# Optimization experiments

Measured on AMD Instinct MI355X. Metric: run time of the kernel, lower is better.

## Reference

```python
import jax, jax.numpy as jnp
import numpy as np
import math

D_MODEL = 1024
N_HEADS = 16
D_K = D_MODEL // N_HEADS


def setup_inputs() -> dict:
    key = jax.random.key(0)
    ks = jax.random.split(key, 12)
    B, S, D = 4, 2048, D_MODEL
    scale = 1.0 / math.sqrt(D)
    inp = {
        "q": jax.random.normal(ks[0], (B, S, D), jnp.float32),
        "k": jax.random.normal(ks[1], (B, S, D), jnp.float32),
        "v": jax.random.normal(ks[2], (B, S, D), jnp.float32),
        "w_q": jax.random.normal(ks[3], (D, D), jnp.float32) * scale,
        "b_q": jnp.zeros((D,), jnp.float32),
        "w_k": jax.random.normal(ks[4], (D, D), jnp.float32) * scale,
        "b_k": jnp.zeros((D,), jnp.float32),
        "w_v": jax.random.normal(ks[5], (D, D), jnp.float32) * scale,
        "b_v": jnp.zeros((D,), jnp.float32),
        "w_o": jax.random.normal(ks[6], (D, D), jnp.float32) * scale,
        "b_o": jnp.zeros((D,), jnp.float32),
        "ln_gamma": jnp.ones((D,), jnp.float32),
        "ln_beta": jnp.zeros((D,), jnp.float32),
    }
    return inp


def reference(q, k, v, w_q, b_q, w_k, b_k, w_v, b_v, w_o, b_o, ln_gamma, ln_beta):
    B, Sq, D = q.shape
    Sk = k.shape[1]
    residual = q
    # Projections (torch Linear: x @ W.T + b); split into heads -> [B, H, S, d_k]
    qh = (q @ w_q.T + b_q).reshape(B, Sq, N_HEADS, D_K).transpose(0, 2, 1, 3)
    kh = (k @ w_k.T + b_k).reshape(B, Sk, N_HEADS, D_K).transpose(0, 2, 1, 3)
    vh = (v @ w_v.T + b_v).reshape(B, Sk, N_HEADS, D_K).transpose(0, 2, 1, 3)
    # Scaled dot-product attention (dropout is identity in eval mode)
    scores = jnp.einsum("bhqd,bhkd->bhqk", qh, kh) / jnp.sqrt(jnp.float32(D_K))
    attn = jax.nn.softmax(scores, axis=-1)  # [B, H, Sq, Sk]
    ctx = jnp.einsum("bhqk,bhkd->bhqd", attn, vh)
    ctx = ctx.transpose(0, 2, 1, 3).reshape(B, Sq, D)
    out = ctx @ w_o.T + b_o
    # Post-LN with residual
    x = out + residual
    mu = jnp.mean(x, axis=-1, keepdims=True)
    var = jnp.var(x, axis=-1, keepdims=True)
    out = (x - mu) / jnp.sqrt(var + 1e-5) * ln_gamma + ln_beta
    return out, attn
```

## Files before the change

### kernel.cpp

```cpp
#include <hip/hip_runtime.h>

#define B_ 4
#define S_ 2048
#define D_ 1024
#define H_ 16
#define DK_ 64
#define M_ (B_ * S_)

typedef __attribute__((ext_vector_type(8))) _Float16 f16x8;
typedef __attribute__((ext_vector_type(4))) _Float16 f16x4;
typedef __attribute__((ext_vector_type(4))) float f32x4;

__device__ __forceinline__ f32x4 mfma16(f16x8 a, f16x8 b, f32x4 c) {
  return __builtin_amdgcn_mfma_f32_16x16x32_f16(a, b, c, 0, 0, 0);
}

__device__ __forceinline__ void gl2lds(const _Float16* g, _Float16* l) {
  __builtin_amdgcn_global_load_lds(
      (const __attribute__((address_space(1))) void*)g,
      (__attribute__((address_space(3))) void*)l, 16, 0, 0);
}

__global__ __launch_bounds__(256) void cvt8(const float* __restrict__ src,
                                            _Float16* __restrict__ dst, int n8) {
  const int i = blockIdx.x * 256 + threadIdx.x;
  if (i >= n8) return;
  const f32x4 a = *reinterpret_cast<const f32x4*>(&src[(size_t)i * 8]);
  const f32x4 b = *reinterpret_cast<const f32x4*>(&src[(size_t)i * 8 + 4]);
  f16x8 h;
  h[0] = (_Float16)a[0]; h[1] = (_Float16)a[1]; h[2] = (_Float16)a[2]; h[3] = (_Float16)a[3];
  h[4] = (_Float16)b[0]; h[5] = (_Float16)b[1]; h[6] = (_Float16)b[2]; h[7] = (_Float16)b[3];
  *reinterpret_cast<f16x8*>(&dst[(size_t)i * 8]) = h;
}

template <int MODE>
__global__ __launch_bounds__(256) void gemm_f16(const _Float16* __restrict__ A,
                                                const _Float16* __restrict__ Bw,
                                                const float* __restrict__ bias,
                                                void* __restrict__ Yv) {
  __shared__ _Float16 As[128 * 64];
  __shared__ _Float16 Bs[128 * 64];
  const int t = threadIdx.x;
  const int lane = t & 63;
  const int w = t >> 6;
  const int wr = w >> 1, wc = w & 1;
  const int l15 = lane & 15, g = lane >> 4;
  const int m0 = (blockIdx.x & 63) * 128;
  const int n0 = (blockIdx.x >> 6) * 128;

  f32x4 acc[4][4] = {};
  const int srow = lane >> 3;
  const int schk = (lane & 7) * 8;

  for (int kt = 0; kt < 16; ++kt) {
    const int k0 = kt * 64;
#pragma unroll
    for (int u = 0; u < 4; ++u) {
      const int r = u * 32 + w * 8 + srow;
      gl2lds(&A[(size_t)(m0 + r) * D_ + k0 + schk], &As[u * 2048 + w * 512]);
      gl2lds(&Bw[(size_t)(n0 + r) * D_ + k0 + schk], &Bs[u * 2048 + w * 512]);
    }
    __syncthreads();
#pragma unroll
    for (int kk = 0; kk < 2; ++kk) {
      f16x8 af[4], bfr[4];
#pragma unroll
      for (int m = 0; m < 4; ++m)
        af[m] = *reinterpret_cast<const f16x8*>(&As[(wr * 64 + m * 16 + l15) * 64 + kk * 32 + 8 * g]);
#pragma unroll
      for (int n = 0; n < 4; ++n)
        bfr[n] = *reinterpret_cast<const f16x8*>(&Bs[(wc * 64 + n * 16 + l15) * 64 + kk * 32 + 8 * g]);
#pragma unroll
      for (int m = 0; m < 4; ++m)
#pragma unroll
        for (int n = 0; n < 4; ++n)
          acc[m][n] = mfma16(af[m], bfr[n], acc[m][n]);
    }
    __syncthreads();
  }

  if constexpr (MODE == 0 || MODE == 1) {
    _Float16* Y = (_Float16*)Yv;
#pragma unroll
    for (int m = 0; m < 4; ++m)
#pragma unroll
      for (int n = 0; n < 4; ++n)
#pragma unroll
        for (int i = 0; i < 4; ++i) {
          const int R = m0 + wr * 64 + m * 16 + 4 * g + i;
          const int C = n0 + wc * 64 + n * 16 + l15;
          float val = acc[m][n][i] + bias[C];
          if constexpr (MODE == 1) val *= 0.125f;
          Y[(size_t)R * D_ + C] = (_Float16)val;
        }
  } else if constexpr (MODE == 2) {
    _Float16* Y = (_Float16*)Yv;
#pragma unroll
    for (int m = 0; m < 4; ++m)
#pragma unroll
      for (int n = 0; n < 4; ++n) {
        const int R0 = m0 + wr * 64 + m * 16 + 4 * g;
        const int C = n0 + wc * 64 + n * 16 + l15;
        const int b = R0 >> 11, s0 = R0 & (S_ - 1);
        const int h = C >> 6, dk = C & (DK_ - 1);
        f16x4 hv;
#pragma unroll
        for (int i = 0; i < 4; ++i) hv[i] = (_Float16)(acc[m][n][i] + bias[C]);
        *reinterpret_cast<f16x4*>(&Y[((size_t)((b * H_ + h) * DK_ + dk)) * S_ + s0]) = hv;
      }
  } else {
    float* Y = (float*)Yv;
#pragma unroll
    for (int m = 0; m < 4; ++m)
#pragma unroll
      for (int n = 0; n < 4; ++n)
#pragma unroll
        for (int i = 0; i < 4; ++i) {
          const int R = m0 + wr * 64 + m * 16 + 4 * g + i;
          const int C = n0 + wc * 64 + n * 16 + l15;
          Y[(size_t)R * D_ + C] = acc[m][n][i] + bias[C];
        }
  }
}

__global__ __launch_bounds__(256) void attn_pass1(const _Float16* __restrict__ Qh,
                                                  const _Float16* __restrict__ Kh,
                                                  float* __restrict__ lbuf) {
  __shared__ float red[4][64];
  const int t = threadIdx.x;
  const int lane = t & 63;
  const int w = t >> 6;
  const int l15 = lane & 15, g = lane >> 4;
  const int qc = blockIdx.x & 31;
  const int bh = blockIdx.x >> 5;
  const int b = bh >> 4, h = bh & 15;
  const int q0 = qc * 64;
  const _Float16* Qp = Qh + (size_t)b * S_ * D_ + h * DK_;
  const _Float16* Kp = Kh + (size_t)b * S_ * D_ + h * DK_;

  f16x8 qa[4][2];
#pragma unroll
  for (int mr = 0; mr < 4; ++mr)
#pragma unroll
    for (int kk = 0; kk < 2; ++kk)
      qa[mr][kk] = *reinterpret_cast<const f16x8*>(&Qp[(size_t)(q0 + mr * 16 + l15) * D_ + kk * 32 + 8 * g]);

  float l[4][4] = {};
  const int cbeg = w * (S_ / 4), cend = cbeg + (S_ / 4);
  for (int c0 = cbeg; c0 < cend; c0 += 16) {
    f16x8 kb0 = *reinterpret_cast<const f16x8*>(&Kp[(size_t)(c0 + l15) * D_ + 8 * g]);
    f16x8 kb1 = *reinterpret_cast<const f16x8*>(&Kp[(size_t)(c0 + l15) * D_ + 32 + 8 * g]);
#pragma unroll
    for (int mr = 0; mr < 4; ++mr) {
      f32x4 sc = {};
      sc = mfma16(qa[mr][0], kb0, sc);
      sc = mfma16(qa[mr][1], kb1, sc);
#pragma unroll
      for (int i = 0; i < 4; ++i) l[mr][i] += __expf(sc[i]);
    }
  }
#pragma unroll
  for (int mask = 1; mask < 16; mask <<= 1)
#pragma unroll
    for (int mr = 0; mr < 4; ++mr)
#pragma unroll
      for (int i = 0; i < 4; ++i) l[mr][i] += __shfl_xor(l[mr][i], mask, 64);
  if (l15 == 0)
#pragma unroll
    for (int mr = 0; mr < 4; ++mr)
#pragma unroll
      for (int i = 0; i < 4; ++i) red[w][mr * 16 + 4 * g + i] = l[mr][i];
  __syncthreads();
  if (t < 64)
    lbuf[(size_t)bh * S_ + q0 + t] = red[0][t] + red[1][t] + red[2][t] + red[3][t];
}

__global__ __launch_bounds__(256) void attn_pass2(const _Float16* __restrict__ Qh,
                                                  const _Float16* __restrict__ Kh,
                                                  const _Float16* __restrict__ Vt,
                                                  const float* __restrict__ lbuf,
                                                  float* __restrict__ attn,
                                                  _Float16* __restrict__ ctx) {
  __shared__ float Ps[4][32 * 36];
  const int t = threadIdx.x;
  const int lane = t & 63;
  const int w = t >> 6;
  const int l15 = lane & 15, g = lane >> 4;
  const int qc = blockIdx.x & 15;
  const int bh = blockIdx.x >> 4;
  const int b = bh >> 4, h = bh & 15;
  const int q0 = qc * 128 + w * 32;
  const _Float16* Qp = Qh + (size_t)b * S_ * D_ + h * DK_;
  const _Float16* Kp = Kh + (size_t)b * S_ * D_ + h * DK_;
  const _Float16* Vp = Vt + (size_t)bh * DK_ * S_;

  f16x8 qa[2][2];
#pragma unroll
  for (int mr = 0; mr < 2; ++mr)
#pragma unroll
    for (int kk = 0; kk < 2; ++kk)
      qa[mr][kk] = *reinterpret_cast<const f16x8*>(&Qp[(size_t)(q0 + mr * 16 + l15) * D_ + kk * 32 + 8 * g]);

  float il[2][4];
#pragma unroll
  for (int mr = 0; mr < 2; ++mr)
#pragma unroll
    for (int i = 0; i < 4; ++i)
      il[mr][i] = 1.0f / lbuf[(size_t)bh * S_ + q0 + mr * 16 + 4 * g + i];

  f32x4 accv[2][4] = {};
  float* Pw = Ps[w];
  const int sr = lane >> 3;
  const int sc4 = (lane & 7) * 4;

  for (int c0 = 0; c0 < S_; c0 += 32) {
#pragma unroll
    for (int ct = 0; ct < 2; ++ct) {
      const f16x8 kb0 = *reinterpret_cast<const f16x8*>(&Kp[(size_t)(c0 + ct * 16 + l15) * D_ + 8 * g]);
      const f16x8 kb1 = *reinterpret_cast<const f16x8*>(&Kp[(size_t)(c0 + ct * 16 + l15) * D_ + 32 + 8 * g]);
#pragma unroll
      for (int mr = 0; mr < 2; ++mr) {
        f32x4 sc = {};
        sc = mfma16(qa[mr][0], kb0, sc);
        sc = mfma16(qa[mr][1], kb1, sc);
#pragma unroll
        for (int i = 0; i < 4; ++i)
          Pw[(mr * 16 + 4 * g + i) * 36 + ct * 16 + l15] = __expf(sc[i]) * il[mr][i];
      }
    }
#pragma unroll
    for (int j = 0; j < 4; ++j) {
      const int r = sr + 8 * j;
      const f32x4 pv = *reinterpret_cast<const f32x4*>(&Pw[r * 36 + sc4]);
      __builtin_nontemporal_store(pv,
          reinterpret_cast<f32x4*>(&attn[((size_t)bh * S_ + q0 + r) * S_ + c0 + sc4]));
    }
#pragma unroll
    for (int mr = 0; mr < 2; ++mr) {
      const f32x4 p0 = *reinterpret_cast<const f32x4*>(&Pw[(mr * 16 + l15) * 36 + 8 * g]);
      const f32x4 p1 = *reinterpret_cast<const f32x4*>(&Pw[(mr * 16 + l15) * 36 + 8 * g + 4]);
      f16x8 pa;
#pragma unroll
      for (int j = 0; j < 4; ++j) { pa[j] = (_Float16)p0[j]; pa[4 + j] = (_Float16)p1[j]; }
#pragma unroll
      for (int n = 0; n < 4; ++n) {
        const f16x8 vb = *reinterpret_cast<const f16x8*>(&Vp[(size_t)(n * 16 + l15) * S_ + c0 + 8 * g]);
        accv[mr][n] = mfma16(pa, vb, accv[mr][n]);
      }
    }
  }
#pragma unroll
  for (int mr = 0; mr < 2; ++mr)
#pragma unroll
    for (int n = 0; n < 4; ++n)
#pragma unroll
      for (int i = 0; i < 4; ++i) {
        const int row = q0 + mr * 16 + 4 * g + i;
        ctx[((size_t)(b * S_ + row)) * D_ + h * DK_ + n * 16 + l15] = (_Float16)accv[mr][n][i];
      }
}

__global__ __launch_bounds__(256) void ln_kernel(float* __restrict__ out,
                                                 const float* __restrict__ resid,
                                                 const float* __restrict__ gamma,
                                                 const float* __restrict__ beta) {
  __shared__ float red[8];
  const int row = blockIdx.x;
  const int t = threadIdx.x;
  const int lane = t & 63, w = t >> 6;
  const size_t base = (size_t)row * D_ + t * 4;
  const f32x4 o = *reinterpret_cast<const f32x4*>(&out[base]);
  const f32x4 r = *reinterpret_cast<const f32x4*>(&resid[base]);
  const f32x4 x = o + r;
  float s = x[0] + x[1] + x[2] + x[3];
  float s2 = x[0] * x[0] + x[1] * x[1] + x[2] * x[2] + x[3] * x[3];
#pragma unroll
  for (int mask = 1; mask < 64; mask <<= 1) {
    s += __shfl_xor(s, mask, 64);
    s2 += __shfl_xor(s2, mask, 64);
  }
  if (lane == 0) { red[w] = s; red[w + 4] = s2; }
  __syncthreads();
  s = red[0] + red[1] + red[2] + red[3];
  s2 = red[4] + red[5] + red[6] + red[7];
  const float mu = s * (1.0f / D_);
  const float var = s2 * (1.0f / D_) - mu * mu;
  const float rstd = rsqrtf(var + 1e-5f);
  const f32x4 gm = *reinterpret_cast<const f32x4*>(&gamma[t * 4]);
  const f32x4 bt = *reinterpret_cast<const f32x4*>(&beta[t * 4]);
  f32x4 y;
#pragma unroll
  for (int j = 0; j < 4; ++j) y[j] = (x[j] - mu) * rstd * gm[j] + bt[j];
  *reinterpret_cast<f32x4*>(&out[base]) = y;
}

extern "C" void kernel_launch(void* const* d_in, const int* in_sizes, int n_in,
                              void* d_out, int out_size, void* d_ws, size_t ws_size,
                              hipStream_t stream) {
  (void)in_sizes; (void)n_in; (void)out_size; (void)ws_size;
  const float* q    = (const float*)d_in[0];
  const float* k    = (const float*)d_in[1];
  const float* v    = (const float*)d_in[2];
  const float* w_q  = (const float*)d_in[3];
  const float* b_q  = (const float*)d_in[4];
  const float* w_k  = (const float*)d_in[5];
  const float* b_k  = (const float*)d_in[6];
  const float* w_v  = (const float*)d_in[7];
  const float* b_v  = (const float*)d_in[8];
  const float* w_o  = (const float*)d_in[9];
  const float* b_o  = (const float*)d_in[10];
  const float* ln_g = (const float*)d_in[11];
  const float* ln_b = (const float*)d_in[12];

  char* ws = (char*)d_ws;
  _Float16* wq_h = (_Float16*)(ws + ((size_t)0 << 20));
  _Float16* wk_h = (_Float16*)(ws + ((size_t)2 << 20));
  _Float16* wv_h = (_Float16*)(ws + ((size_t)4 << 20));
  _Float16* wo_h = (_Float16*)(ws + ((size_t)6 << 20));
  _Float16* qf   = (_Float16*)(ws + ((size_t)8 << 20));
  _Float16* kf   = (_Float16*)(ws + ((size_t)26 << 20));
  _Float16* vf   = (_Float16*)(ws + ((size_t)44 << 20));
  _Float16* Qh   = (_Float16*)(ws + ((size_t)62 << 20));
  _Float16* Kh   = (_Float16*)(ws + ((size_t)80 << 20));
  _Float16* Vt   = (_Float16*)(ws + ((size_t)98 << 20));
  _Float16* ctx  = (_Float16*)(ws + ((size_t)116 << 20));
  float*    lbuf = (float*)(ws + ((size_t)134 << 20));

  float* out_f = (float*)d_out;
  float* attn_f = out_f + (size_t)M_ * D_;

  const int n8in = M_ * D_ / 8;
  const int n8w  = D_ * D_ / 8;
  cvt8<<<n8in / 256, 256, 0, stream>>>(q, qf, n8in);
  cvt8<<<n8in / 256, 256, 0, stream>>>(k, kf, n8in);
  cvt8<<<n8in / 256, 256, 0, stream>>>(v, vf, n8in);
  cvt8<<<n8w / 256, 256, 0, stream>>>(w_q, wq_h, n8w);
  cvt8<<<n8w / 256, 256, 0, stream>>>(w_k, wk_h, n8w);
  cvt8<<<n8w / 256, 256, 0, stream>>>(w_v, wv_h, n8w);
  cvt8<<<n8w / 256, 256, 0, stream>>>(w_o, wo_h, n8w);

  gemm_f16<1><<<512, 256, 0, stream>>>(qf, wq_h, b_q, Qh);
  gemm_f16<0><<<512, 256, 0, stream>>>(kf, wk_h, b_k, Kh);
  gemm_f16<2><<<512, 256, 0, stream>>>(vf, wv_h, b_v, Vt);

  attn_pass1<<<B_ * H_ * (S_ / 64), 256, 0, stream>>>(Qh, Kh, lbuf);
  attn_pass2<<<B_ * H_ * (S_ / 128), 256, 0, stream>>>(Qh, Kh, Vt, lbuf, attn_f, ctx);

  gemm_f16<3><<<512, 256, 0, stream>>>(ctx, wo_h, b_o, out_f);
  ln_kernel<<<M_, 256, 0, stream>>>(out_f, q, ln_g, ln_b);
}
```

Before: 541.2 us.

## Fuse softmax denominator pass into attention kernel and merge conversion launches

Folds the row-sum pass into the attention kernel: each wave first sweeps all keys to accumulate exp sums for its 32 query rows, then runs the existing probability/context pass, removing the separate kernel and the lbuf round trip. The seven fp32-to-fp16 conversion launches are merged into one indexed kernel. The Q scale now includes log2(e) so exp2f replaces __expf. The fused kernel has fewer blocks per row-sum sweep (32 rows per wave instead of 64 per block split across waves), so the first pass has less parallelism and more redundant K reads.

Result: slower. 614.6 us (+13.5%).

```diff
diff --git a/kernel.cpp b/kernel.cpp
--- a/kernel.cpp
+++ b/kernel.cpp
@@ -11,6 +11,8 @@
 typedef __attribute__((ext_vector_type(4))) _Float16 f16x4;
 typedef __attribute__((ext_vector_type(4))) float f32x4;
 
+#define QSCALE 0.18033688011113607f
+
 __device__ __forceinline__ f32x4 mfma16(f16x8 a, f16x8 b, f32x4 c) {
   return __builtin_amdgcn_mfma_f32_16x16x32_f16(a, b, c, 0, 0, 0);
 }
@@ -21,16 +23,37 @@
       (__attribute__((address_space(3))) void*)l, 16, 0, 0);
 }
 
-__global__ __launch_bounds__(256) void cvt8(const float* __restrict__ src,
-                                            _Float16* __restrict__ dst, int n8) {
+#define NIN8 (M_ * D_ / 8)
+#define NW8 (D_ * D_ / 8)
+__global__ __launch_bounds__(256) void cvt_all(
+    const float* __restrict__ q, const float* __restrict__ k, const float* __restrict__ v,
+    const float* __restrict__ wq, const float* __restrict__ wk, const float* __restrict__ wv,
+    const float* __restrict__ wo,
+    _Float16* __restrict__ qf, _Float16* __restrict__ kf, _Float16* __restrict__ vf,
+    _Float16* __restrict__ wqh, _Float16* __restrict__ wkh, _Float16* __restrict__ wvh,
+    _Float16* __restrict__ woh) {
   const int i = blockIdx.x * 256 + threadIdx.x;
-  if (i >= n8) return;
-  const f32x4 a = *reinterpret_cast<const f32x4*>(&src[(size_t)i * 8]);
-  const f32x4 b = *reinterpret_cast<const f32x4*>(&src[(size_t)i * 8 + 4]);
+  const float* src;
+  _Float16* dst;
+  int off;
+  if (i < 3 * NIN8) {
+    const int t = i >> 20;
+    off = i & (NIN8 - 1);
+    src = t == 0 ? q : (t == 1 ? k : v);
+    dst = t == 0 ? qf : (t == 1 ? kf : vf);
+  } else {
+    const int j = i - 3 * NIN8;
+    const int t = j >> 17;
+    off = j & (NW8 - 1);
+    src = t == 0 ? wq : (t == 1 ? wk : (t == 2 ? wv : wo));
+    dst = t == 0 ? wqh : (t == 1 ? wkh : (t == 2 ? wvh : woh));
+  }
+  const f32x4 a = *reinterpret_cast<const f32x4*>(&src[(size_t)off * 8]);
+  const f32x4 b = *reinterpret_cast<const f32x4*>(&src[(size_t)off * 8 + 4]);
   f16x8 h;
   h[0] = (_Float16)a[0]; h[1] = (_Float16)a[1]; h[2] = (_Float16)a[2]; h[3] = (_Float16)a[3];
   h[4] = (_Float16)b[0]; h[5] = (_Float16)b[1]; h[6] = (_Float16)b[2]; h[7] = (_Float16)b[3];
-  *reinterpret_cast<f16x8*>(&dst[(size_t)i * 8]) = h;
+  *reinterpret_cast<f16x8*>(&dst[(size_t)off * 8]) = h;
 }
 
 template <int MODE>
@@ -90,7 +113,7 @@
           const int R = m0 + wr * 64 + m * 16 + 4 * g + i;
           const int C = n0 + wc * 64 + n * 16 + l15;
           float val = acc[m][n][i] + bias[C];
-          if constexpr (MODE == 1) val *= 0.125f;
+          if constexpr (MODE == 1) val *= QSCALE;
           Y[(size_t)R * D_ + C] = (_Float16)val;
         }
   } else if constexpr (MODE == 2) {
@@ -123,62 +146,9 @@
   }
 }
 
-__global__ __launch_bounds__(256) void attn_pass1(const _Float16* __restrict__ Qh,
-                                                  const _Float16* __restrict__ Kh,
-                                                  float* __restrict__ lbuf) {
-  __shared__ float red[4][64];
-  const int t = threadIdx.x;
-  const int lane = t & 63;
-  const int w = t >> 6;
-  const int l15 = lane & 15, g = lane >> 4;
-  const int qc = blockIdx.x & 31;
-  const int bh = blockIdx.x >> 5;
-  const int b = bh >> 4, h = bh & 15;
-  const int q0 = qc * 64;
-  const _Float16* Qp = Qh + (size_t)b * S_ * D_ + h * DK_;
-  const _Float16* Kp = Kh + (size_t)b * S_ * D_ + h * DK_;
-
-  f16x8 qa[4][2];
-#pragma unroll
-  for (int mr = 0; mr < 4; ++mr)
-#pragma unroll
-    for (int kk = 0; kk < 2; ++kk)
-      qa[mr][kk] = *reinterpret_cast<const f16x8*>(&Qp[(size_t)(q0 + mr * 16 + l15) * D_ + kk * 32 + 8 * g]);
-
-  float l[4][4] = {};
-  const int cbeg = w * (S_ / 4), cend = cbeg + (S_ / 4);
-  for (int c0 = cbeg; c0 < cend; c0 += 16) {
-    f16x8 kb0 = *reinterpret_cast<const f16x8*>(&Kp[(size_t)(c0 + l15) * D_ + 8 * g]);
-    f16x8 kb1 = *reinterpret_cast<const f16x8*>(&Kp[(size_t)(c0 + l15) * D_ + 32 + 8 * g]);
-#pragma unroll
-    for (int mr = 0; mr < 4; ++mr) {
-      f32x4 sc = {};
-      sc = mfma16(qa[mr][0], kb0, sc);
-      sc = mfma16(qa[mr][1], kb1, sc);
-#pragma unroll
-      for (int i = 0; i < 4; ++i) l[mr][i] += __expf(sc[i]);
-    }
-  }
-#pragma unroll
-  for (int mask = 1; mask < 16; mask <<= 1)
-#pragma unroll
-    for (int mr = 0; mr < 4; ++mr)
-#pragma unroll
-      for (int i = 0; i < 4; ++i) l[mr][i] += __shfl_xor(l[mr][i], mask, 64);
-  if (l15 == 0)
-#pragma unroll
-    for (int mr = 0; mr < 4; ++mr)
-#pragma unroll
-      for (int i = 0; i < 4; ++i) red[w][mr * 16 + 4 * g + i] = l[mr][i];
-  __syncthreads();
-  if (t < 64)
-    lbuf[(size_t)bh * S_ + q0 + t] = red[0][t] + red[1][t] + red[2][t] + red[3][t];
-}
-
-__global__ __launch_bounds__(256) void attn_pass2(const _Float16* __restrict__ Qh,
+__global__ __launch_bounds__(256) void attn_fused(const _Float16* __restrict__ Qh,
                                                   const _Float16* __restrict__ Kh,
                                                   const _Float16* __restrict__ Vt,
-                                                  const float* __restrict__ lbuf,
                                                   float* __restrict__ attn,
                                                   _Float16* __restrict__ ctx) {
   __shared__ float Ps[4][32 * 36];
@@ -201,12 +171,30 @@
     for (int kk = 0; kk < 2; ++kk)
       qa[mr][kk] = *reinterpret_cast<const f16x8*>(&Qp[(size_t)(q0 + mr * 16 + l15) * D_ + kk * 32 + 8 * g]);
 
+  float l[2][4] = {};
+  for (int c0 = 0; c0 < S_; c0 += 16) {
+    const f16x8 kb0 = *reinterpret_cast<const f16x8*>(&Kp[(size_t)(c0 + l15) * D_ + 8 * g]);
+    const f16x8 kb1 = *reinterpret_cast<const f16x8*>(&Kp[(size_t)(c0 + l15) * D_ + 32 + 8 * g]);
+#pragma unroll
+    for (int mr = 0; mr < 2; ++mr) {
+      f32x4 sc = {};
+      sc = mfma16(qa[mr][0], kb0, sc);
+      sc = mfma16(qa[mr][1], kb1, sc);
+#pragma unroll
+      for (int i = 0; i < 4; ++i) l[mr][i] += exp2f(sc[i]);
+    }
+  }
+#pragma unroll
+  for (int mask = 1; mask < 16; mask <<= 1)
+#pragma unroll
+    for (int mr = 0; mr < 2; ++mr)
+#pragma unroll
+      for (int i = 0; i < 4; ++i) l[mr][i] += __shfl_xor(l[mr][i], mask, 64);
   float il[2][4];
 #pragma unroll
   for (int mr = 0; mr < 2; ++mr)
 #pragma unroll
-    for (int i = 0; i < 4; ++i)
-      il[mr][i] = 1.0f / lbuf[(size_t)bh * S_ + q0 + mr * 16 + 4 * g + i];
+    for (int i = 0; i < 4; ++i) il[mr][i] = 1.0f / l[mr][i];
 
   f32x4 accv[2][4] = {};
   float* Pw = Ps[w];
@@ -225,7 +213,7 @@
         sc = mfma16(qa[mr][1], kb1, sc);
 #pragma unroll
         for (int i = 0; i < 4; ++i)
-          Pw[(mr * 16 + 4 * g + i) * 36 + ct * 16 + l15] = __expf(sc[i]) * il[mr][i];
+          Pw[(mr * 16 + 4 * g + i) * 36 + ct * 16 + l15] = exp2f(sc[i]) * il[mr][i];
       }
     }
 #pragma unroll
@@ -324,27 +312,18 @@
   _Float16* Kh   = (_Float16*)(ws + ((size_t)80 << 20));
   _Float16* Vt   = (_Float16*)(ws + ((size_t)98 << 20));
   _Float16* ctx  = (_Float16*)(ws + ((size_t)116 << 20));
-  float*    lbuf = (float*)(ws + ((size_t)134 << 20));
 
   float* out_f = (float*)d_out;
   float* attn_f = out_f + (size_t)M_ * D_;
 
-  const int n8in = M_ * D_ / 8;
-  const int n8w  = D_ * D_ / 8;
-  cvt8<<<n8in / 256, 256, 0, stream>>>(q, qf, n8in);
-  cvt8<<<n8in / 256, 256, 0, stream>>>(k, kf, n8in);
-  cvt8<<<n8in / 256, 256, 0, stream>>>(v, vf, n8in);
-  cvt8<<<n8w / 256, 256, 0, stream>>>(w_q, wq_h, n8w);
-  cvt8<<<n8w / 256, 256, 0, stream>>>(w_k, wk_h, n8w);
-  cvt8<<<n8w / 256, 256, 0, stream>>>(w_v, wv_h, n8w);
-  cvt8<<<n8w / 256, 256, 0, stream>>>(w_o, wo_h, n8w);
+  cvt_all<<<(3 * NIN8 + 4 * NW8) / 256, 256, 0, stream>>>(
+      q, k, v, w_q, w_k, w_v, w_o, qf, kf, vf, wq_h, wk_h, wv_h, wo_h);
 
   gemm_f16<1><<<512, 256, 0, stream>>>(qf, wq_h, b_q, Qh);
   gemm_f16<0><<<512, 256, 0, stream>>>(kf, wk_h, b_k, Kh);
   gemm_f16<2><<<512, 256, 0, stream>>>(vf, wv_h, b_v, Vt);
 
-  attn_pass1<<<B_ * H_ * (S_ / 64), 256, 0, stream>>>(Qh, Kh, lbuf);
-  attn_pass2<<<B_ * H_ * (S_ / 128), 256, 0, stream>>>(Qh, Kh, Vt, lbuf, attn_f, ctx);
+  attn_fused<<<B_ * H_ * (S_ / 128), 256, 0, stream>>>(Qh, Kh, Vt, attn_f, ctx);
 
   gemm_f16<3><<<512, 256, 0, stream>>>(ctx, wo_h, b_o, out_f);
   ln_kernel<<<M_, 256, 0, stream>>>(out_f, q, ln_g, ln_b);
```

## Fuse fp32-to-fp16 input conversion into a single batched QKV projection GEMM

Applied to the files above, without the earlier changes.

The three activation conversion kernels are removed. The Q/K/V projections become one 1536-block GEMM launch that loads fp32 activations and converts them to fp16 while staging them into padded LDS. The four weight conversions are merged into one kernel, and Q is pre-scaled by log2(e)/8 so the softmax can use exp2f in place of __expf. This saves the fp16 intermediate round trip through memory and several launches, but the A-tile path now uses register loads instead of the async global-to-LDS copy.

Result: faster. 509.5 us (-5.9%).

```diff
diff --git a/kernel.cpp b/kernel.cpp
--- a/kernel.cpp
+++ b/kernel.cpp
@@ -11,6 +11,8 @@
 typedef __attribute__((ext_vector_type(4))) _Float16 f16x4;
 typedef __attribute__((ext_vector_type(4))) float f32x4;
 
+#define QSCALE 0.18033688011113607f
+
 __device__ __forceinline__ f32x4 mfma16(f16x8 a, f16x8 b, f32x4 c) {
   return __builtin_amdgcn_mfma_f32_16x16x32_f16(a, b, c, 0, 0, 0);
 }
@@ -21,23 +23,119 @@
       (__attribute__((address_space(3))) void*)l, 16, 0, 0);
 }
 
-__global__ __launch_bounds__(256) void cvt8(const float* __restrict__ src,
-                                            _Float16* __restrict__ dst, int n8) {
+#define NW8 (D_ * D_ / 8)
+__global__ __launch_bounds__(256) void cvt_w(
+    const float* __restrict__ wq, const float* __restrict__ wk,
+    const float* __restrict__ wv, const float* __restrict__ wo,
+    _Float16* __restrict__ wqh, _Float16* __restrict__ wkh,
+    _Float16* __restrict__ wvh, _Float16* __restrict__ woh) {
   const int i = blockIdx.x * 256 + threadIdx.x;
-  if (i >= n8) return;
-  const f32x4 a = *reinterpret_cast<const f32x4*>(&src[(size_t)i * 8]);
-  const f32x4 b = *reinterpret_cast<const f32x4*>(&src[(size_t)i * 8 + 4]);
+  const int t = i >> 17;
+  const int off = i & (NW8 - 1);
+  const float* src = t == 0 ? wq : (t == 1 ? wk : (t == 2 ? wv : wo));
+  _Float16* dst = t == 0 ? wqh : (t == 1 ? wkh : (t == 2 ? wvh : woh));
+  const f32x4 a = *reinterpret_cast<const f32x4*>(&src[(size_t)off * 8]);
+  const f32x4 b = *reinterpret_cast<const f32x4*>(&src[(size_t)off * 8 + 4]);
   f16x8 h;
   h[0] = (_Float16)a[0]; h[1] = (_Float16)a[1]; h[2] = (_Float16)a[2]; h[3] = (_Float16)a[3];
   h[4] = (_Float16)b[0]; h[5] = (_Float16)b[1]; h[6] = (_Float16)b[2]; h[7] = (_Float16)b[3];
-  *reinterpret_cast<f16x8*>(&dst[(size_t)i * 8]) = h;
-}
-
-template <int MODE>
-__global__ __launch_bounds__(256) void gemm_f16(const _Float16* __restrict__ A,
+  *reinterpret_cast<f16x8*>(&dst[(size_t)off * 8]) = h;
+}
+
+__global__ __launch_bounds__(256) void gemm_qkv(
+    const float* __restrict__ Xq, const float* __restrict__ Xk, const float* __restrict__ Xv,
+    const _Float16* __restrict__ Wq, const _Float16* __restrict__ Wk, const _Float16* __restrict__ Wv,
+    const float* __restrict__ bq, const float* __restrict__ bk, const float* __restrict__ bv,
+    _Float16* __restrict__ Qh, _Float16* __restrict__ Kh, _Float16* __restrict__ Vt) {
+  __shared__ _Float16 As[128 * 72];
+  __shared__ _Float16 Bs[128 * 64];
+  const int third = blockIdx.x >> 9;
+  const int bid = blockIdx.x & 511;
+  const float* X = third == 0 ? Xq : (third == 1 ? Xk : Xv);
+  const _Float16* Bw = third == 0 ? Wq : (third == 1 ? Wk : Wv);
+  const float* bias = third == 0 ? bq : (third == 1 ? bk : bv);
+
+  const int t = threadIdx.x;
+  const int lane = t & 63;
+  const int w = t >> 6;
+  const int wr = w >> 1, wc = w & 1;
+  const int l15 = lane & 15, g = lane >> 4;
+  const int m0 = (bid & 63) * 128;
+  const int n0 = (bid >> 6) * 128;
+
+  f32x4 acc[4][4] = {};
+  const int srow = lane >> 3;
+  const int schk = (lane & 7) * 8;
+  const int ar = t >> 4;
+  const int ac = (t & 15) * 4;
+
+  for (int kt = 0; kt < 16; ++kt) {
+    const int k0 = kt * 64;
+#pragma unroll
+    for (int u = 0; u < 4; ++u)
+      gl2lds(&Bw[(size_t)(n0 + u * 32 + w * 8 + srow) * D_ + k0 + schk], &Bs[u * 2048 + w * 512]);
+#pragma unroll
+    for (int rg = 0; rg < 8; ++rg) {
+      const int r = rg * 16 + ar;
+      const f32x4 vv = *reinterpret_cast<const f32x4*>(&X[(size_t)(m0 + r) * D_ + k0 + ac]);
+      f16x4 hh;
+      hh[0] = (_Float16)vv[0]; hh[1] = (_Float16)vv[1];
+      hh[2] = (_Float16)vv[2]; hh[3] = (_Float16)vv[3];
+      *reinterpret_cast<f16x4*>(&As[r * 72 + ac]) = hh;
+    }
+    __syncthreads();
+#pragma unroll
+    for (int kk = 0; kk < 2; ++kk) {
+      f16x8 af[4], bfr[4];
+#pragma unroll
+      for (int m = 0; m < 4; ++m)
+        af[m] = *reinterpret_cast<const f16x8*>(&As[(wr * 64 + m * 16 + l15) * 72 + kk * 32 + 8 * g]);
+#pragma unroll
+      for (int n = 0; n < 4; ++n)
+        bfr[n] = *reinterpret_cast<const f16x8*>(&Bs[(wc * 64 + n * 16 + l15) * 64 + kk * 32 + 8 * g]);
+#pragma unroll
+      for (int m = 0; m < 4; ++m)
+#pragma unroll
+        for (int n = 0; n < 4; ++n)
+          acc[m][n] = mfma16(af[m], bfr[n], acc[m][n]);
+    }
+    __syncthreads();
+  }
+
+  if (third < 2) {
+    _Float16* Y = third == 0 ? Qh : Kh;
+    const float scl = third == 0 ? QSCALE : 1.0f;
+#pragma unroll
+    for (int m = 0; m < 4; ++m)
+#pragma unroll
+      for (int n = 0; n < 4; ++n)
+#pragma unroll
+        for (int i = 0; i < 4; ++i) {
+          const int R = m0 + wr * 64 + m * 16 + 4 * g + i;
+          const int C = n0 + wc * 64 + n * 16 + l15;
+          Y[(size_t)R * D_ + C] = (_Float16)((acc[m][n][i] + bias[C]) * scl);
+        }
+  } else {
+#pragma unroll
+    for (int m = 0; m < 4; ++m)
+#pragma unroll
+      for (int n = 0; n < 4; ++n) {
+        const int R0 = m0 + wr * 64 + m * 16 + 4 * g;
+        const int C = n0 + wc * 64 + n * 16 + l15;
+        const int b = R0 >> 11, s0 = R0 & (S_ - 1);
+        const int h = C >> 6, dk = C & (DK_ - 1);
+        f16x4 hv;
+#pragma unroll
+        for (int i = 0; i < 4; ++i) hv[i] = (_Float16)(acc[m][n][i] + bias[C]);
+        *reinterpret_cast<f16x4*>(&Vt[((size_t)((b * H_ + h) * DK_ + dk)) * S_ + s0]) = hv;
+      }
+  }
+}
+
+__global__ __launch_bounds__(256) void gemm_out(const _Float16* __restrict__ A,
                                                 const _Float16* __restrict__ Bw,
                                                 const float* __restrict__ bias,
-                                                void* __restrict__ Yv) {
+                                                float* __restrict__ out) {
   __shared__ _Float16 As[128 * 64];
   __shared__ _Float16 Bs[128 * 64];
   const int t = threadIdx.x;
@@ -79,48 +177,16 @@
     __syncthreads();
   }
 
-  if constexpr (MODE == 0 || MODE == 1) {
-    _Float16* Y = (_Float16*)Yv;
-#pragma unroll
-    for (int m = 0; m < 4; ++m)
-#pragma unroll
-      for (int n = 0; n < 4; ++n)
-#pragma unroll
-        for (int i = 0; i < 4; ++i) {
-          const int R = m0 + wr * 64 + m * 16 + 4 * g + i;
-          const int C = n0 + wc * 64 + n * 16 + l15;
-          float val = acc[m][n][i] + bias[C];
-          if constexpr (MODE == 1) val *= 0.125f;
-          Y[(size_t)R * D_ + C] = (_Float16)val;
-        }
-  } else if constexpr (MODE == 2) {
-    _Float16* Y = (_Float16*)Yv;
-#pragma unroll
-    for (int m = 0; m < 4; ++m)
-#pragma unroll
-      for (int n = 0; n < 4; ++n) {
-        const int R0 = m0 + wr * 64 + m * 16 + 4 * g;
+#pragma unroll
+  for (int m = 0; m < 4; ++m)
+#pragma unroll
+    for (int n = 0; n < 4; ++n)
+#pragma unroll
+      for (int i = 0; i < 4; ++i) {
+        const int R = m0 + wr * 64 + m * 16 + 4 * g + i;
         const int C = n0 + wc * 64 + n * 16 + l15;
-        const int b = R0 >> 11, s0 = R0 & (S_ - 1);
-        const int h = C >> 6, dk = C & (DK_ - 1);
-        f16x4 hv;
-#pragma unroll
-        for (int i = 0; i < 4; ++i) hv[i] = (_Float16)(acc[m][n][i] + bias[C]);
-        *reinterpret_cast<f16x4*>(&Y[((size_t)((b * H_ + h) * DK_ + dk)) * S_ + s0]) = hv;
+        out[(size_t)R * D_ + C] = acc[m][n][i] + bias[C];
       }
-  } else {
-    float* Y = (float*)Yv;
-#pragma unroll
-    for (int m = 0; m < 4; ++m)
-#pragma unroll
-      for (int n = 0; n < 4; ++n)
-#pragma unroll
-        for (int i = 0; i < 4; ++i) {
-          const int R = m0 + wr * 64 + m * 16 + 4 * g + i;
-          const int C = n0 + wc * 64 + n * 16 + l15;
-          Y[(size_t)R * D_ + C] = acc[m][n][i] + bias[C];
-        }
-  }
 }
 
 __global__ __launch_bounds__(256) void attn_pass1(const _Float16* __restrict__ Qh,
@@ -148,15 +214,15 @@
   float l[4][4] = {};
   const int cbeg = w * (S_ / 4), cend = cbeg + (S_ / 4);
   for (int c0 = cbeg; c0 < cend; c0 += 16) {
-    f16x8 kb0 = *reinterpret_cast<const f16x8*>(&Kp[(size_t)(c0 + l15) * D_ + 8 * g]);
-    f16x8 kb1 = *reinterpret_cast<const f16x8*>(&Kp[(size_t)(c0 + l15) * D_ + 32 + 8 * g]);
+    const f16x8 kb0 = *reinterpret_cast<const f16x8*>(&Kp[(size_t)(c0 + l15) * D_ + 8 * g]);
+    const f16x8 kb1 = *reinterpret_cast<const f16x8*>(&Kp[(size_t)(c0 + l15) * D_ + 32 + 8 * g]);
 #pragma unroll
     for (int mr = 0; mr < 4; ++mr) {
       f32x4 sc = {};
       sc = mfma16(qa[mr][0], kb0, sc);
       sc = mfma16(qa[mr][1], kb1, sc);
 #pragma unroll
-      for (int i = 0; i < 4; ++i) l[mr][i] += __expf(sc[i]);
+      for (int i = 0; i < 4; ++i) l[mr][i] += exp2f(sc[i]);
     }
   }
 #pragma unroll
@@ -225,7 +291,7 @@
         sc = mfma16(qa[mr][1], kb1, sc);
 #pragma unroll
         for (int i = 0; i < 4; ++i)
-          Pw[(mr * 16 + 4 * g + i) * 36 + ct * 16 + l15] = __expf(sc[i]) * il[mr][i];
+          Pw[(mr * 16 + 4 * g + i) * 36 + ct * 16 + l15] = exp2f(sc[i]) * il[mr][i];
       }
     }
 #pragma unroll
@@ -317,35 +383,22 @@
   _Float16* wk_h = (_Float16*)(ws + ((size_t)2 << 20));
   _Float16* wv_h = (_Float16*)(ws + ((size_t)4 << 20));
   _Float16* wo_h = (_Float16*)(ws + ((size_t)6 << 20));
-  _Float16* qf   = (_Float16*)(ws + ((size_t)8 << 20));
-  _Float16* kf   = (_Float16*)(ws + ((size_t)26 << 20));
-  _Float16* vf   = (_Float16*)(ws + ((size_t)44 << 20));
-  _Float16* Qh   = (_Float16*)(ws + ((size_t)62 << 20));
-  _Float16* Kh   = (_Float16*)(ws + ((size_t)80 << 20));
-  _Float16* Vt   = (_Float16*)(ws + ((size_t)98 << 20));
-  _Float16* ctx  = (_Float16*)(ws + ((size_t)116 << 20));
-  float*    lbuf = (float*)(ws + ((size_t)134 << 20));
+  _Float16* Qh   = (_Float16*)(ws + ((size_t)8 << 20));
+  _Float16* Kh   = (_Float16*)(ws + ((size_t)26 << 20));
+  _Float16* Vt   = (_Float16*)(ws + ((size_t)44 << 20));
+  _Float16* ctx  = (_Float16*)(ws + ((size_t)62 << 20));
+  float*    lbuf = (float*)(ws + ((size_t)80 << 20));
 
   float* out_f = (float*)d_out;
   float* attn_f = out_f + (size_t)M_ * D_;
 
-  const int n8in = M_ * D_ / 8;
-  const int n8w  = D_ * D_ / 8;
-  cvt8<<<n8in / 256, 256, 0, stream>>>(q, qf, n8in);
-  cvt8<<<n8in / 256, 256, 0, stream>>>(k, kf, n8in);
-  cvt8<<<n8in / 256, 256, 0, stream>>>(v, vf, n8in);
-  cvt8<<<n8w / 256, 256, 0, stream>>>(w_q, wq_h, n8w);
-  cvt8<<<n8w / 256, 256, 0, stream>>>(w_k, wk_h, n8w);
-  cvt8<<<n8w / 256, 256, 0, stream>>>(w_v, wv_h, n8w);
-  cvt8<<<n8w / 256, 256, 0, stream>>>(w_o, wo_h, n8w);
-
-  gemm_f16<1><<<512, 256, 0, stream>>>(qf, wq_h, b_q, Qh);
-  gemm_f16<0><<<512, 256, 0, stream>>>(kf, wk_h, b_k, Kh);
-  gemm_f16<2><<<512, 256, 0, stream>>>(vf, wv_h, b_v, Vt);
+  cvt_w<<<4 * NW8 / 256, 256, 0, stream>>>(w_q, w_k, w_v, w_o, wq_h, wk_h, wv_h, wo_h);
+
+  gemm_qkv<<<1536, 256, 0, stream>>>(q, k, v, wq_h, wk_h, wv_h, b_q, b_k, b_v, Qh, Kh, Vt);
 
   attn_pass1<<<B_ * H_ * (S_ / 64), 256, 0, stream>>>(Qh, Kh, lbuf);
   attn_pass2<<<B_ * H_ * (S_ / 128), 256, 0, stream>>>(Qh, Kh, Vt, lbuf, attn_f, ctx);
 
-  gemm_f16<3><<<512, 256, 0, stream>>>(ctx, wo_h, b_o, out_f);
+  gemm_out<<<512, 256, 0, stream>>>(ctx, wo_h, b_o, out_f);
   ln_kernel<<<M_, 256, 0, stream>>>(out_f, q, ln_g, ln_b);
 }
```
